# Optimization experiments

Hardware: AMD Instinct MI355X
Metric: run time of the kernel (lower is better)

Reference implementation:

```python
import jax, jax.numpy as jnp
import numpy as np

N, E = 16384, 65536
N2, A2, E2 = 65536, 131072, 262144
N3, A3, E3 = 65536, 196608, 262144
B = 256
F_IN, NI2, NI3 = 16, 64, 64


def setup_inputs() -> dict:
    key = jax.random.key(0)
    ks = iter(jax.random.split(key, 80))
    def rn(shape, s=1.0):
        return jax.random.normal(next(ks), shape, jnp.float32) * s
    def ru(shape):
        return jax.random.uniform(next(ks), shape, dtype=jnp.float32)
    def ri(shape, hi):
        return jax.random.randint(next(ks), shape, 0, hi)
    s = 0.05
    inp = {
        "x": rn((N, F_IN)),
        "edge_index": ri((2, E), N),
        "edge_attr": ru((E, 7)),
        "batch": jnp.sort(ri((N,), B)),
        "assign2_node": ri((A2,), N),
        "assign2_cluster": ri((A2,), N2),
        "iso_type_2": ru((N2, NI2)),
        "edge_index_2": ri((2, E2), N2),
        "batch_2": jnp.sort(ri((N2,), B)),
        "assign3_node": ri((A3,), N),
        "assign3_cluster": ri((A3,), N3),
        "iso_type_3": ru((N3, NI3)),
        "edge_index_3": ri((2, E3), N3),
        "batch_3": jnp.sort(ri((N3,), B)),
    }
    for i, (mi, mo) in enumerate([(F_IN, 32), (32, 64), (64, 64)], start=1):
        inp[f"nn{i}_W1"] = rn((7, 128), s)
        inp[f"nn{i}_b1"] = jnp.zeros((128,), jnp.float32)
        inp[f"nn{i}_W2"] = rn((128, mi * mo), s)
        inp[f"nn{i}_b2"] = jnp.zeros((mi * mo,), jnp.float32)
        inp[f"conv{i}_root"] = rn((mi, mo), s)
        inp[f"conv{i}_bias"] = jnp.zeros((mo,), jnp.float32)
    for i, din in zip([4, 5, 6, 7], [64 + NI2, 64, 64 + NI3, 64]):
        inp[f"conv{i}_Wrel"] = rn((din, 64), s)
        inp[f"conv{i}_Wroot"] = rn((din, 64), s)
        inp[f"conv{i}_bias"] = jnp.zeros((64,), jnp.float32)
    inp["fc1_W"] = rn((384, 64), s); inp["fc1_b"] = jnp.zeros((64,), jnp.float32)
    inp["fc2_W"] = rn((64, 32), s); inp["fc2_b"] = jnp.zeros((32,), jnp.float32)
    inp["fc3_W"] = rn((32, 1), s); inp["fc3_b"] = jnp.zeros((1,), jnp.float32)
    return inp


def nnconv(x, ei, ea, W1, b1, W2, b2, root, bias, mi, mo):
    # edge MLP -> per-edge [mi, mo] weight matrix; message = x_src @ W_e; scatter-add to dst
    h = jax.nn.relu(ea @ W1 + b1) @ W2 + b2          # [E, mi*mo]
    We = h.reshape(-1, mi, mo)
    msg = jnp.einsum('ei,eio->eo', x[ei[0]], We)     # [E, mo]
    agg = jax.ops.segment_sum(msg, ei[1], num_segments=x.shape[0])
    return x @ root + agg + bias


def graphconv(x, ei, Wrel, Wroot, bias):
    agg = jax.ops.segment_sum(x[ei[0]], ei[1], num_segments=x.shape[0])
    return agg @ Wrel + x @ Wroot + bias


def avg_pool_assign(x, node_idx, cluster_idx, num_clusters):
    s = jax.ops.segment_sum(x[node_idx], cluster_idx, num_segments=num_clusters)
    c = jax.ops.segment_sum(jnp.ones((node_idx.shape[0],), x.dtype), cluster_idx, num_segments=num_clusters)
    return s / jnp.clip(c, 1.0)[:, None]


def reference(x, edge_index, edge_attr, batch, assign2_node, assign2_cluster, iso_type_2, edge_index_2, batch_2, assign3_node, assign3_cluster, iso_type_3, edge_index_3, batch_3, nn1_W1, nn1_b1, nn1_W2, nn1_b2, conv1_root, conv1_bias, nn2_W1, nn2_b1, nn2_W2, nn2_b2, conv2_root, conv2_bias, nn3_W1, nn3_b1, nn3_W2, nn3_b2, conv3_root, conv3_bias, conv4_Wrel, conv4_Wroot, conv4_bias, conv5_Wrel, conv5_Wroot, conv5_bias, conv6_Wrel, conv6_Wroot, conv6_bias, conv7_Wrel, conv7_Wroot, conv7_bias, fc1_W, fc1_b, fc2_W, fc2_b, fc3_W, fc3_b):
    elu = jax.nn.elu
    h = elu(nnconv(x, edge_index, edge_attr, nn1_W1, nn1_b1, nn1_W2, nn1_b2, conv1_root, conv1_bias, F_IN, 32))
    h = elu(nnconv(h, edge_index, edge_attr, nn2_W1, nn2_b1, nn2_W2, nn2_b2, conv2_root, conv2_bias, 32, 64))
    h = elu(nnconv(h, edge_index, edge_attr, nn3_W1, nn3_b1, nn3_W2, nn3_b2, conv3_root, conv3_bias, 64, 64))
    x_1 = jax.ops.segment_sum(h, batch, num_segments=B)
    # 2-set level
    h2 = avg_pool_assign(h, assign2_node, assign2_cluster, N2)
    h2 = jnp.concatenate([h2, iso_type_2], axis=1)
    h2 = elu(graphconv(h2, edge_index_2, conv4_Wrel, conv4_Wroot, conv4_bias))
    h2 = elu(graphconv(h2, edge_index_2, conv5_Wrel, conv5_Wroot, conv5_bias))
    x_2 = jax.ops.segment_sum(h2, batch_2, num_segments=B)
    # 3-set level
    h3 = avg_pool_assign(h, assign3_node, assign3_cluster, N3)
    h3 = jnp.concatenate([h3, iso_type_3], axis=1)
    h3 = elu(graphconv(h3, edge_index_3, conv6_Wrel, conv6_Wroot, conv6_bias))
    h3 = elu(graphconv(h3, edge_index_3, conv7_Wrel, conv7_Wroot, conv7_bias))
    x_3 = jax.ops.segment_sum(h3, batch_3, num_segments=B)
    xc = jnp.concatenate([x_1, x_2, x_3], axis=1)
    xc = jnp.concatenate([xc, xc], axis=1)      # [B, 384]
    o = elu(xc @ fc1_W + fc1_b)
    o = elu(o @ fc2_W + fc2_b)
    o = o @ fc3_W + fc3_b
    return o.reshape(-1)
```

## Files before the change

### kernel.cpp

```cpp
#include <hip/hip_runtime.h>
#include <math.h>

#define NN 16384
#define E1N 65536
#define NBATCH 256
#define NC2 65536
#define KH 128
#define MNSTR 1092
#define OCS 136
#define ECAP 96

typedef _Float16 f16;
typedef _Float16 f16x2 __attribute__((ext_vector_type(2)));
typedef _Float16 f16x4 __attribute__((ext_vector_type(4)));
typedef _Float16 f16x8 __attribute__((ext_vector_type(8)));
typedef float    f32x4 __attribute__((ext_vector_type(4)));

__device__ __forceinline__ float elu1(float x){ return x > 0.f ? x : expm1f(x); }

__device__ __forceinline__ float dot2acc(f16x2 a, f16x2 b, float c){
#if __has_builtin(__builtin_amdgcn_fdot2)
  return __builtin_amdgcn_fdot2(a, b, c, false);
#else
  return fmaf((float)a[0], (float)b[0], fmaf((float)a[1], (float)b[1], c));
#endif
}

__global__ __launch_bounds__(256) void k_count(const int* __restrict__ arr, int* __restrict__ cnt, int n){
  int i = blockIdx.x*256 + threadIdx.x;
  if (i < n) atomicAdd(&cnt[arr[i]], 1);
}

__global__ __launch_bounds__(256) void k_scan1(const int* __restrict__ deg,
    int* __restrict__ ptr, int* __restrict__ partials){
  __shared__ int buf[256];
  int i = blockIdx.x*256 + threadIdx.x, t = threadIdx.x;
  int v = deg[i];
  buf[t] = v; __syncthreads();
  for (int o = 1; o < 256; o <<= 1){
    int x = (t >= o) ? buf[t-o] : 0;
    __syncthreads(); buf[t] += x; __syncthreads();
  }
  ptr[i] = buf[t] - v;
  if (t == 255) partials[blockIdx.x] = buf[255];
}

__global__ __launch_bounds__(256) void k_scan2(int* __restrict__ partials, int nb){
  __shared__ int buf[256];
  int t = threadIdx.x;
  int v = (t < nb) ? partials[t] : 0;
  buf[t] = v; __syncthreads();
  for (int o = 1; o < 256; o <<= 1){
    int x = (t >= o) ? buf[t-o] : 0;
    __syncthreads(); buf[t] += x; __syncthreads();
  }
  if (t < nb) partials[t] = buf[t] - v;
}

__global__ __launch_bounds__(256) void k_scan3(const int* __restrict__ partials,
    int* __restrict__ ptr, int* __restrict__ cur){
  int i = blockIdx.x*256 + threadIdx.x;
  int v = ptr[i] + partials[blockIdx.x];
  ptr[i] = v; cur[i] = v;
}

__global__ __launch_bounds__(256) void k_fill_edge(const int* __restrict__ ei, int* __restrict__ cursor,
    int* __restrict__ eids, int* __restrict__ srcs, int* __restrict__ dsts){
  int e = blockIdx.x*256 + threadIdx.x;
  if (e >= E1N) return;
  int s = ei[e];
  int p = atomicAdd(&cursor[s], 1);
  eids[p] = e; srcs[p] = s; dsts[p] = ei[E1N + e];
}

__global__ __launch_bounds__(256) void k_fill_dst(const int* __restrict__ eiL, int* __restrict__ cur,
    int* __restrict__ dsrc, int EL){
  int e = blockIdx.x*256 + threadIdx.x;
  if (e >= EL) return;
  int d = eiL[EL + e];
  int p = atomicAdd(&cur[d], 1);
  dsrc[p] = eiL[e];
}

__global__ __launch_bounds__(256) void k_fill_assign(const int* __restrict__ an, const int* __restrict__ ac,
    int* __restrict__ cur, int* __restrict__ an_sorted, int A){
  int a = blockIdx.x*256 + threadIdx.x;
  if (a >= A) return;
  int c = ac[a];
  int p = atomicAdd(&cur[c], 1);
  an_sorted[p] = an[a];
}

__global__ __launch_bounds__(256) void k_cvt16(const float* __restrict__ v, f16* __restrict__ o, int n){
  int t = blockIdx.x*256 + threadIdx.x;
  if (t < n) o[t] = (f16)v[t];
}

__global__ __launch_bounds__(256) void k_elu_both(float* __restrict__ v, f16* __restrict__ v16, int n){
  int t = blockIdx.x*256 + threadIdx.x;
  if (t < n){ float r = elu1(v[t]); v[t] = r; v16[t] = (f16)r; }
}

__global__ __launch_bounds__(256) void k_elu(float* __restrict__ v, int n){
  int t = blockIdx.x*256 + threadIdx.x;
  if (t < n) v[t] = elu1(v[t]);
}

__global__ __launch_bounds__(256) void k_packPrep(const float* __restrict__ root,
    const float* __restrict__ b2, f16* __restrict__ Bp, int mi, int mo, int S, int NB){
  int t = blockIdx.x*256 + threadIdx.x;
  if (t >= NB*S*512) return;
  int j = t & 7, l = (t >> 3) & 63, cs = t >> 9;
  int s = cs % S, c = cs / S;
  int k_in = s*32 + ((l>>4)<<3) + j;
  int n = c*16 + (l & 15);
  float v = 0.f;
  if (k_in < mi) v = (n < mo) ? root[k_in*mo + n] : b2[k_in*mo + (n - mo)];
  Bp[t] = (f16)v;
}

template<int MI, int S, int NB, int MO>
__global__ __launch_bounds__(256) void k_prep_mfma(const f16* __restrict__ A,
    const f16* __restrict__ Bp, const float* __restrict__ bias,
    float* __restrict__ outb, float* __restrict__ bterm){
  int l = threadIdx.x & 63, w = threadIdx.x >> 6;
  int r0 = blockIdx.x*64 + w*16;
  const f16* arow = A + (size_t)(r0 + (l & 15))*MI;
  f16x8 a[S];
  #pragma unroll
  for (int s=0;s<S;s++){
    int koff = s*32 + ((l>>4)<<3);
    if (koff < MI) a[s] = *(const f16x8*)(arow + koff);
    else           a[s] = (f16x8){0,0,0,0,0,0,0,0};
  }
  #pragma unroll
  for (int c=0;c<NB;c++){
    f32x4 acc = (f32x4){0.f,0.f,0.f,0.f};
    #pragma unroll
    for (int s=0;s<S;s++){
      f16x8 b = *(const f16x8*)(Bp + ((size_t)(c*S + s)*64 + l)*8);
      acc = __builtin_amdgcn_mfma_f32_16x16x32_f16(a[s], b, acc, 0, 0, 0);
    }
    int col = c*16 + (l & 15);
    #pragma unroll
    for (int r=0;r<4;r++){
      int row = r0 + ((l>>4)<<2) + r;
      if (col < MO) outb[(size_t)row*MO + col] = acc[r] + bias[col];
      else          bterm[(size_t)row*MO + (col - MO)] = acc[r];
    }
  }
}

__global__ __launch_bounds__(256) void k_w2pack_full(const float* __restrict__ W2,
    f16* __restrict__ Bp, int mi, int mo, int S){
  int t = blockIdx.x*256 + threadIdx.x;
  if (t >= mo*8*S*512) return;
  int j = t & 7, l = (t >> 3) & 63, cs = t >> 9;
  int s = cs % S, q = cs / S;
  int oc = q >> 3;
  int k  = (q & 7)*16 + (l & 15);
  int i  = s*32 + ((l>>4)<<3) + j;
  float v = (i < mi) ? W2[(size_t)k*mi*mo + (size_t)i*mo + oc] : 0.f;
  Bp[t] = (f16)v;
}

template<int MI, int S, int MO>
__global__ __launch_bounds__(256) void k_nnconv_fused3(const f16* __restrict__ xin16,
    const f16* __restrict__ W2p,
    const int* __restrict__ rowptr, const int* __restrict__ rowend,
    const int* __restrict__ srcs, const int* __restrict__ dsts,
    const int* __restrict__ eids,
    const float* __restrict__ ea, const float* __restrict__ W1,
    const float* __restrict__ b1,
    const float* __restrict__ bterm, float* __restrict__ outb){
  __shared__ __align__(16) f16   M[16*MNSTR];
  __shared__ __align__(16) f16   hb[ECAP*OCS];
  __shared__ __align__(16) float eas[ECAP*8];
  int t = threadIdx.x, l = t & 63, w = t >> 6;
  int n0 = blockIdx.x*16;
  int estart = rowptr[n0], eend = rowend[n0+15];
  if (estart >= eend) return;
  const f16* arow = xin16 + (size_t)(n0 + (l&15))*MI;
  f16x8 a[S];
  #pragma unroll
  for (int s=0;s<S;s++){
    int koff = s*32 + ((l>>4)<<3);
    if (koff < MI) a[s] = *(const f16x8*)(arow + koff);
    else           a[s] = (f16x8){0,0,0,0,0,0,0,0};
  }
  const int NCHUNK = MO/8;
  int oc = t & 7, eslot = t >> 3;
  for (int ebase = estart; ebase < eend; ebase += ECAP){
    int ecnt = eend - ebase; if (ecnt > ECAP) ecnt = ECAP;
    for (int idx = t; idx < ecnt*8; idx += 256){
      int e_ = idx >> 3, i = idx & 7;
      eas[idx] = (i < 7) ? ea[(size_t)eids[ebase + e_]*7 + i] : 0.f;
    }
    __syncthreads();
    for (int idx = t; idx < ecnt*32; idx += 256){
      int e_ = idx >> 5, p = idx & 31;
      int k0 = p*4;
      const float* xr = &eas[e_*8];
      float4 acc4 = *(const float4*)(b1 + k0);
      #pragma unroll
      for (int i=0;i<7;i++){
        float xv = xr[i];
        float4 wv = *(const float4*)(W1 + i*KH + k0);
        acc4.x = fmaf(xv, wv.x, acc4.x);
        acc4.y = fmaf(xv, wv.y, acc4.y);
        acc4.z = fmaf(xv, wv.z, acc4.z);
        acc4.w = fmaf(xv, wv.w, acc4.w);
      }
      f16x4 hv = { (f16)fmaxf(acc4.x,0.f), (f16)fmaxf(acc4.y,0.f),
                   (f16)fmaxf(acc4.z,0.f), (f16)fmaxf(acc4.w,0.f) };
      *(f16x4*)&hb[e_*OCS + k0] = hv;
    }
    __syncthreads();
    for (int c = 0; c < NCHUNK; c++){
      #pragma unroll
      for (int tt = 0; tt < 16; tt++){
        int q = c*64 + w*16 + tt;
        f32x4 acc = (f32x4){0.f,0.f,0.f,0.f};
        #pragma unroll
        for (int s=0;s<S;s++){
          f16x8 b = *(const f16x8*)(W2p + ((size_t)(q*S + s)*64 + l)*8);
          acc = __builtin_amdgcn_mfma_f32_16x16x32_f16(a[s], b, acc, 0, 0, 0);
        }
        int ocl = w*2 + (tt>>3);
        int kpos = (tt&7)*16 + (l & 15);
        f16* mp = &M[ocl*OCS + kpos];
        #pragma unroll
        for (int r=0;r<4;r++)
          mp[(size_t)(((l>>4)<<2) + r)*MNSTR] = (f16)acc[r];
      }
      __syncthreads();
      #pragma unroll
      for (int r2 = 0; r2 < ECAP/32; r2++){
        int ee = r2*32 + eslot;
        if (ee < ecnt){
          int e = ebase + ee;
          int s_ = srcs[e];
          int ln = s_ - n0;
          float acc = bterm[(size_t)s_*MO + c*8 + oc];
          const f16* mrow = &M[(size_t)ln*MNSTR + oc*OCS];
          const f16* hrow = &hb[ee*OCS];
          #pragma unroll 4
          for (int kk=0; kk<16; kk++){
            f16x8 h8 = *(const f16x8*)(hrow + kk*8);
            f16x4 m0 = *(const f16x4*)(mrow + kk*8);
            f16x4 m1 = *(const f16x4*)(mrow + kk*8 + 4);
            acc = dot2acc((f16x2){h8[0],h8[1]}, (f16x2){m0[0],m0[1]}, acc);
            acc = dot2acc((f16x2){h8[2],h8[3]}, (f16x2){m0[2],m0[3]}, acc);
            acc = dot2acc((f16x2){h8[4],h8[5]}, (f16x2){m1[0],m1[1]}, acc);
            acc = dot2acc((f16x2){h8[6],h8[7]}, (f16x2){m1[2],m1[3]}, acc);
          }
          atomicAdd(&outb[(size_t)dsts[e]*MO + c*8 + oc], acc);
        }
      }
      __syncthreads();
    }
  }
}

__global__ __launch_bounds__(256) void k_pool_gather(const int* __restrict__ aptr,
    const int* __restrict__ aend, const int* __restrict__ an_sorted,
    const float* __restrict__ h, const float* __restrict__ iso,
    f16* __restrict__ h16){
  int l = threadIdx.x & 63, w = threadIdx.x >> 6;
  int c = blockIdx.x*4 + w;
  int st = aptr[c], en = aend[c];
  float acc = 0.f;
  int e = st;
  for (; e+1 < en; e += 2){
    int n0 = an_sorted[e], n1 = an_sorted[e+1];
    acc += h[(size_t)n0*64 + l];
    acc += h[(size_t)n1*64 + l];
  }
  if (e < en) acc += h[(size_t)an_sorted[e]*64 + l];
  int cnt = en - st;
  float val = (cnt > 0) ? acc / (float)cnt : 0.f;
  h16[(size_t)c*128 + l] = (f16)val;
  h16[(size_t)c*128 + 64 + l] = (f16)iso[(size_t)c*64 + l];
}

__global__ __launch_bounds__(256) void k_packB_gc(const float* __restrict__ Wrel,
    const float* __restrict__ Wroot, f16* __restrict__ Bp, int S){
  int t = blockIdx.x*256 + threadIdx.x;
  if (t >= 8*S*512) return;
  int j = t & 7, l = (t >> 3) & 63, cs = t >> 9;
  int s = cs % S, c = cs / S;
  int k = s*32 + ((l>>4)<<3) + j;
  int n = (c<<4) + (l & 15);
  float v = (n < 64) ? Wrel[k*64 + n] : Wroot[k*64 + (n - 64)];
  Bp[t] = (f16)v;
}

template<int S>
__global__ __launch_bounds__(256) void k_gc_mfma(const f16* __restrict__ A,
    const f16* __restrict__ Bp, const float* __restrict__ bias,
    float* __restrict__ y, float* __restrict__ rbuf){
  int l = threadIdx.x & 63, w = threadIdx.x >> 6;
  int r0 = blockIdx.x*64 + w*16;
  const f16* arow = A + (size_t)(r0 + (l & 15))*(S*32);
  f16x8 a[S];
  #pragma unroll
  for (int s=0;s<S;s++) a[s] = *(const f16x8*)(arow + s*32 + ((l>>4)<<3));
  f32x4 acc[8];
  #pragma unroll
  for (int c=0;c<8;c++) acc[c] = (f32x4){0.f,0.f,0.f,0.f};
  #pragma unroll
  for (int c=0;c<8;c++){
    #pragma unroll
    for (int s=0;s<S;s++){
      f16x8 b = *(const f16x8*)(Bp + ((size_t)(c*S + s)*64 + l)*8);
      acc[c] = __builtin_amdgcn_mfma_f32_16x16x32_f16(a[s], b, acc[c], 0, 0, 0);
    }
  }
  #pragma unroll
  for (int c=0;c<8;c++){
    int col = c*16 + (l & 15);
    #pragma unroll
    for (int r=0;r<4;r++){
      int row = r0 + ((l>>4)<<2) + r;
      if (col < 64) y[(size_t)row*64 + col] = acc[c][r];
      else          rbuf[(size_t)row*64 + (col-64)] = acc[c][r] + bias[col-64];
    }
  }
}

template<bool F16OUT>
__global__ __launch_bounds__(256) void k_gc_gather(const int* __restrict__ dptr,
    const int* __restrict__ dend, const int* __restrict__ dsrc,
    const float* __restrict__ y, const float* __restrict__ rbuf,
    f16* __restrict__ o16, float* __restrict__ o32){
  int l = threadIdx.x & 63, w = threadIdx.x >> 6;
  int n = blockIdx.x*4 + w;
  int st = dptr[n], en = dend[n];
  float acc = rbuf[(size_t)n*64 + l];
  int e = st;
  for (; e+1 < en; e += 2){
    int s0 = dsrc[e], s1 = dsrc[e+1];
    acc += y[(size_t)s0*64 + l];
    acc += y[(size_t)s1*64 + l];
  }
  if (e < en) acc += y[(size_t)dsrc[e]*64 + l];
  float r = elu1(acc);
  if (F16OUT) o16[(size_t)n*64 + l] = (f16)r;
  else        o32[(size_t)n*64 + l] = r;
}

__device__ __forceinline__ int lowerb(const int* __restrict__ a, int n, int key){
  int lo = 0, hi = n;
  while (lo < hi){ int m = (lo + hi) >> 1; if (a[m] < key) lo = m + 1; else hi = m; }
  return lo;
}

__global__ __launch_bounds__(256) void k_batchsum_seg(const int* __restrict__ batch,
    const float* __restrict__ h, float* __restrict__ x123, int n_nodes, int off){
  __shared__ float red[4][64];
  int b = blockIdx.x;
  int lo = lowerb(batch, n_nodes, b);
  int hi = lowerb(batch, n_nodes, b+1);
  int col = threadIdx.x & 63, wq = threadIdx.x >> 6;
  float acc = 0.f;
  for (int n = lo + wq; n < hi; n += 4) acc += h[(size_t)n*64 + col];
  red[wq][col] = acc;
  __syncthreads();
  if (threadIdx.x < 64){
    float s = red[0][threadIdx.x] + red[1][threadIdx.x] + red[2][threadIdx.x] + red[3][threadIdx.x];
    x123[b*192 + off + threadIdx.x] = s;
  }
}

__global__ __launch_bounds__(256) void k_fc1(const float* __restrict__ x123,
    const float* __restrict__ W, const float* __restrict__ b, float* __restrict__ t1){
  int t = blockIdx.x*256 + threadIdx.x;
  if (t >= NBATCH*64) return;
  int bb = t >> 6, o = t & 63;
  const float* xr = x123 + bb*192;
  float acc = b[o];
  for (int j=0;j<192;j++) acc = fmaf(xr[j], W[j*64+o] + W[(192+j)*64+o], acc);
  t1[t] = elu1(acc);
}

__global__ __launch_bounds__(256) void k_fc2(const float* __restrict__ t1,
    const float* __restrict__ W, const float* __restrict__ b, float* __restrict__ t2){
  int t = blockIdx.x*256 + threadIdx.x;
  if (t >= NBATCH*32) return;
  int bb = t >> 5, o = t & 31;
  float acc = b[o];
  for (int j=0;j<64;j++) acc = fmaf(t1[bb*64+j], W[j*32+o], acc);
  t2[t] = elu1(acc);
}

__global__ __launch_bounds__(256) void k_fc3(const float* __restrict__ t2,
    const float* __restrict__ W, const float* __restrict__ b, float* __restrict__ out){
  int t = blockIdx.x*256 + threadIdx.x;
  if (t >= NBATCH) return;
  float acc = b[0];
  for (int j=0;j<32;j++) acc = fmaf(t2[t*32+j], W[j], acc);
  out[t] = acc;
}

static inline int cdiv(long long a, int b){ return (int)((a + b - 1) / b); }

extern "C" void kernel_launch(void* const* d_in, const int* in_sizes, int n_in,
                              void* d_out, int out_size, void* d_ws, size_t ws_size,
                              hipStream_t stream) {
  const float* x0    = (const float*)d_in[0];
  const int*   ei    = (const int*)d_in[1];
  const float* ea    = (const float*)d_in[2];
  const int*   batch = (const int*)d_in[3];
  const int*   a2n   = (const int*)d_in[4];
  const int*   a2c   = (const int*)d_in[5];
  const float* iso2  = (const float*)d_in[6];
  const int*   ei2   = (const int*)d_in[7];
  const int*   b2arr = (const int*)d_in[8];
  const int*   a3n   = (const int*)d_in[9];
  const int*   a3c   = (const int*)d_in[10];
  const float* iso3  = (const float*)d_in[11];
  const int*   ei3   = (const int*)d_in[12];
  const int*   b3arr = (const int*)d_in[13];
  const float* nnp[3][6];
  for (int c=0;c<3;c++) for (int p=0;p<6;p++) nnp[c][p] = (const float*)d_in[14 + 6*c + p];
  const float* c4W[3]; const float* c5W[3]; const float* c6W[3]; const float* c7W[3];
  for (int p=0;p<3;p++){ c4W[p]=(const float*)d_in[32+p]; c5W[p]=(const float*)d_in[35+p];
                         c6W[p]=(const float*)d_in[38+p]; c7W[p]=(const float*)d_in[41+p]; }
  const float* fc1W=(const float*)d_in[44]; const float* fc1b=(const float*)d_in[45];
  const float* fc2W=(const float*)d_in[46]; const float* fc2b=(const float*)d_in[47];
  const float* fc3W=(const float*)d_in[48]; const float* fc3b=(const float*)d_in[49];
  float* outp = (float*)d_out;

  char* ws = (char*)d_ws; size_t off = 0;
  auto alloc = [&](size_t bytes)->void*{ void* p = ws + off; off += (bytes + 255) & ~(size_t)255; return p; };
  const size_t SZ_R0 = (size_t)92*1024*1024;
  char* r0 = (char*)alloc(SZ_R0);
  f16*   W2p   = (f16*)r0;
  f16*   prepB = (f16*)(r0 + 2*1024*1024);
  float* bterm = (float*)(r0 + 2*1024*1024 + 64*1024);
  size_t o2 = 0;
  auto a2 = [&](size_t bytes)->char*{ char* p = r0 + o2; o2 += (bytes + 255) & ~(size_t)255; return p; };
  f16*   h16   = (f16*)  a2((size_t)NC2*128*2);
  float* ybuf  = (float*)a2((size_t)NC2*64*4);
  float* rbuf  = (float*)a2((size_t)NC2*64*4);
  float* gB    = (float*)a2((size_t)NC2*64*4);
  f16*   g16   = (f16*)  a2((size_t)NC2*64*2);
  f16*   BpGc  = (f16*)  a2((size_t)8*4*512*2);
  int*   aptr  = (int*)  a2((size_t)NC2*4);
  int*   acur  = (int*)  a2((size_t)NC2*4);
  int*   dptr  = (int*)  a2((size_t)NC2*4);
  int*   dcur  = (int*)  a2((size_t)NC2*4);
  int*   ldeg  = (int*)  a2((size_t)NC2*4);
  int*   ans   = (int*)  a2((size_t)196608*4);
  int*   dsrc  = (int*)  a2((size_t)262144*4);
  float* hA    = (float*)alloc((size_t)NN*32*4);
  float* hB    = (float*)alloc((size_t)NN*64*4);
  float* hC    = (float*)alloc((size_t)NN*64*4);
  f16*   x016  = (f16*)  alloc((size_t)NN*16*2);
  f16*   hA16  = (f16*)  alloc((size_t)NN*32*2);
  f16*   hB16  = (f16*)  alloc((size_t)NN*64*2);
  int*   deg   = (int*)  alloc((size_t)NN*4);
  int*   cursor= (int*)  alloc((size_t)NN*4);
  int*   rowptr= (int*)  alloc((size_t)NN*4);
  int*   eids  = (int*)  alloc((size_t)E1N*4);
  int*   srcs  = (int*)  alloc((size_t)E1N*4);
  int*   dsts  = (int*)  alloc((size_t)E1N*4);
  int*   parts = (int*)  alloc((size_t)256*4);
  float* x123  = (float*)alloc((size_t)NBATCH*192*4);
  float* t1    = (float*)alloc((size_t)NBATCH*64*4);
  float* t2    = (float*)alloc((size_t)NBATCH*32*4);
  (void)ws_size; (void)n_in; (void)in_sizes; (void)out_size;

  auto scan = [&](const int* dg, int n, int* ptr, int* cur){
    k_scan1<<<n/256,256,0,stream>>>(dg, ptr, parts);
    k_scan2<<<1,256,0,stream>>>(parts, n/256);
    k_scan3<<<n/256,256,0,stream>>>(parts, ptr, cur);
  };

  hipMemsetAsync(deg, 0, (size_t)NN*4, stream);
  k_count<<<cdiv(E1N,256),256,0,stream>>>(ei, deg, E1N);
  scan(deg, NN, rowptr, cursor);
  k_fill_edge<<<cdiv(E1N,256),256,0,stream>>>(ei, cursor, eids, srcs, dsts);
  k_cvt16<<<cdiv((long long)NN*16,256),256,0,stream>>>(x0, x016, NN*16);

  auto run_nnconv = [&](const f16* xin16, int mi, int mo,
                        const float* const* P, float* outb, f16* out16){
    const float* W1=P[0]; const float* b1=P[1]; const float* W2=P[2];
    const float* b2=P[3]; const float* root=P[4]; const float* bias=P[5];
    const int S = (mi > 32) ? 2 : 1;
    const int NB = (2*mo)/16;
    k_packPrep<<<cdiv((long long)NB*S*512,256),256,0,stream>>>(root, b2, prepB, mi, mo, S, NB);
    if (mi==16)      k_prep_mfma<16,1,4,32><<<NN/64,256,0,stream>>>(xin16, prepB, bias, outb, bterm);
    else if (mi==32) k_prep_mfma<32,1,8,64><<<NN/64,256,0,stream>>>(xin16, prepB, bias, outb, bterm);
    else             k_prep_mfma<64,2,8,64><<<NN/64,256,0,stream>>>(xin16, prepB, bias, outb, bterm);
    k_w2pack_full<<<cdiv((long long)mo*8*S*512,256),256,0,stream>>>(W2, W2p, mi, mo, S);
    if (mi==16)      k_nnconv_fused3<16,1,32><<<NN/16,256,0,stream>>>(xin16, W2p, rowptr, cursor, srcs, dsts, eids, ea, W1, b1, bterm, outb);
    else if (mi==32) k_nnconv_fused3<32,1,64><<<NN/16,256,0,stream>>>(xin16, W2p, rowptr, cursor, srcs, dsts, eids, ea, W1, b1, bterm, outb);
    else             k_nnconv_fused3<64,2,64><<<NN/16,256,0,stream>>>(xin16, W2p, rowptr, cursor, srcs, dsts, eids, ea, W1, b1, bterm, outb);
    if (out16) k_elu_both<<<cdiv((long long)NN*mo,256),256,0,stream>>>(outb, out16, NN*mo);
    else       k_elu<<<cdiv((long long)NN*mo,256),256,0,stream>>>(outb, NN*mo);
  };
  run_nnconv(x016, 16, 32, nnp[0], hA, hA16);
  run_nnconv(hA16, 32, 64, nnp[1], hB, hB16);
  run_nnconv(hB16, 64, 64, nnp[2], hC, nullptr);

  k_batchsum_seg<<<NBATCH,256,0,stream>>>(batch, hC, x123, NN, 0);

  auto run_level = [&](const int* an, const int* ac, int A, const float* iso,
                       const int* eiL, int EL, const int* batchL,
                       const float* const* cA, const float* const* cB, int off123){
    hipMemsetAsync(ldeg, 0, (size_t)NC2*4, stream);
    k_count<<<cdiv(A,256),256,0,stream>>>(ac, ldeg, A);
    scan(ldeg, NC2, aptr, acur);
    k_fill_assign<<<cdiv(A,256),256,0,stream>>>(an, ac, acur, ans, A);
    hipMemsetAsync(ldeg, 0, (size_t)NC2*4, stream);
    k_count<<<cdiv(EL,256),256,0,stream>>>(eiL + EL, ldeg, EL);
    scan(ldeg, NC2, dptr, dcur);
    k_fill_dst<<<cdiv(EL,256),256,0,stream>>>(eiL, dcur, dsrc, EL);
    k_pool_gather<<<NC2/4,256,0,stream>>>(aptr, acur, ans, hC, iso, h16);
    k_packB_gc<<<cdiv((long long)8*4*512,256),256,0,stream>>>(cA[0], cA[1], BpGc, 4);
    k_gc_mfma<4><<<NC2/64,256,0,stream>>>(h16, BpGc, cA[2], ybuf, rbuf);
    k_gc_gather<true><<<NC2/4,256,0,stream>>>(dptr, dcur, dsrc, ybuf, rbuf, g16, nullptr);
    k_packB_gc<<<cdiv((long long)8*2*512,256),256,0,stream>>>(cB[0], cB[1], BpGc, 2);
    k_gc_mfma<2><<<NC2/64,256,0,stream>>>(g16, BpGc, cB[2], ybuf, rbuf);
    k_gc_gather<false><<<NC2/4,256,0,stream>>>(dptr, dcur, dsrc, ybuf, rbuf, nullptr, gB);
    k_batchsum_seg<<<NBATCH,256,0,stream>>>(batchL, gB, x123, NC2, off123);
  };
  run_level(a2n, a2c, 131072, iso2, ei2, 262144, b2arr, c4W, c5W, 64);
  run_level(a3n, a3c, 196608, iso3, ei3, 262144, b3arr, c6W, c7W, 128);

  k_fc1<<<cdiv((long long)NBATCH*64,256),256,0,stream>>>(x123, fc1W, fc1b, t1);
  k_fc2<<<cdiv((long long)NBATCH*32,256),256,0,stream>>>(t1, fc2W, fc2b, t2);
  k_fc3<<<cdiv(NBATCH,256),256,0,stream>>>(t2, fc3W, fc3b, outp);
}
```

Baseline: 868.3 us.

## Replace atomic scatter with dst-CSR gather, batch levels, and move intermediates to fp16

The NNConv message kernel now writes per-edge fp16 messages instead of doing float atomic adds to destination nodes. A new destination-sorted gather kernel then sums those messages, adds the root term and applies ELU, which removes the separate ELU passes. The 2-set and 3-set levels are merged into dual kernels with combined counting, scanning, packing, GEMM and gather launches, and their intermediates are stored in fp16 to cut memory traffic. The per-node bterm rows are staged in shared memory. The cost is an extra message buffer and gather pass, plus lower precision in the stored intermediates.

```diff
diff --git a/kernel.cpp b/kernel.cpp
--- a/kernel.cpp
+++ b/kernel.cpp
@@ -5,9 +5,12 @@
 #define E1N 65536
 #define NBATCH 256
 #define NC2 65536
+#define A2N 131072
+#define A3N 196608
+#define ELV 262144
 #define KH 128
+#define OCS 136
 #define MNSTR 1092
-#define OCS 136
 #define ECAP 96
 
 typedef _Float16 f16;
@@ -24,11 +27,6 @@
 #else
   return fmaf((float)a[0], (float)b[0], fmaf((float)a[1], (float)b[1], c));
 #endif
-}
-
-__global__ __launch_bounds__(256) void k_count(const int* __restrict__ arr, int* __restrict__ cnt, int n){
-  int i = blockIdx.x*256 + threadIdx.x;
-  if (i < n) atomicAdd(&cnt[arr[i]], 1);
 }
 
 __global__ __launch_bounds__(256) void k_scan1(const int* __restrict__ deg,
@@ -45,16 +43,16 @@
   if (t == 255) partials[blockIdx.x] = buf[255];
 }
 
-__global__ __launch_bounds__(256) void k_scan2(int* __restrict__ partials, int nb){
+__global__ __launch_bounds__(256) void k_scan2seg(int* __restrict__ partials, int nb){
   __shared__ int buf[256];
-  int t = threadIdx.x;
-  int v = (t < nb) ? partials[t] : 0;
+  int t = threadIdx.x, base = blockIdx.x*nb;
+  int v = (t < nb) ? partials[base + t] : 0;
   buf[t] = v; __syncthreads();
   for (int o = 1; o < 256; o <<= 1){
     int x = (t >= o) ? buf[t-o] : 0;
     __syncthreads(); buf[t] += x; __syncthreads();
   }
-  if (t < nb) partials[t] = buf[t] - v;
+  if (t < nb) partials[base + t] = buf[t] - v;
 }
 
 __global__ __launch_bounds__(256) void k_scan3(const int* __restrict__ partials,
@@ -64,46 +62,65 @@
   ptr[i] = v; cur[i] = v;
 }
 
-__global__ __launch_bounds__(256) void k_fill_edge(const int* __restrict__ ei, int* __restrict__ cursor,
-    int* __restrict__ eids, int* __restrict__ srcs, int* __restrict__ dsts){
+__global__ __launch_bounds__(256) void k_count_edge_dual(const int* __restrict__ ei, int* __restrict__ deg){
   int e = blockIdx.x*256 + threadIdx.x;
   if (e >= E1N) return;
-  int s = ei[e];
-  int p = atomicAdd(&cursor[s], 1);
-  eids[p] = e; srcs[p] = s; dsts[p] = ei[E1N + e];
-}
-
-__global__ __launch_bounds__(256) void k_fill_dst(const int* __restrict__ eiL, int* __restrict__ cur,
-    int* __restrict__ dsrc, int EL){
+  atomicAdd(&deg[ei[e]], 1);
+  atomicAdd(&deg[NN + ei[E1N + e]], 1);
+}
+
+__global__ __launch_bounds__(256) void k_fill_edge_dual(const int* __restrict__ ei, int* __restrict__ cur,
+    int* __restrict__ eids, int* __restrict__ srcs, int* __restrict__ dpos){
   int e = blockIdx.x*256 + threadIdx.x;
-  if (e >= EL) return;
-  int d = eiL[EL + e];
-  int p = atomicAdd(&cur[d], 1);
-  dsrc[p] = eiL[e];
-}
-
-__global__ __launch_bounds__(256) void k_fill_assign(const int* __restrict__ an, const int* __restrict__ ac,
-    int* __restrict__ cur, int* __restrict__ an_sorted, int A){
-  int a = blockIdx.x*256 + threadIdx.x;
-  if (a >= A) return;
-  int c = ac[a];
-  int p = atomicAdd(&cur[c], 1);
-  an_sorted[p] = an[a];
+  if (e >= E1N) return;
+  int s = ei[e], d = ei[E1N + e];
+  int p = atomicAdd(&cur[s], 1);
+  eids[p] = e; srcs[p] = s;
+  int p2 = atomicAdd(&cur[NN + d], 1);
+  dpos[p2] = p;
+}
+
+__global__ __launch_bounds__(256) void k_count_assign_dual(const int* __restrict__ a2c,
+    const int* __restrict__ a3c, int* __restrict__ ldegA){
+  int i = blockIdx.x*256 + threadIdx.x;
+  if (i < A2N) atomicAdd(&ldegA[a2c[i]], 1);
+  else if (i < A2N + A3N) atomicAdd(&ldegA[NC2 + a3c[i - A2N]], 1);
+}
+
+__global__ __launch_bounds__(256) void k_fill_assign_dual(const int* __restrict__ a2n,
+    const int* __restrict__ a2c, const int* __restrict__ a3n, const int* __restrict__ a3c,
+    int* __restrict__ curA, int* __restrict__ ans2, int* __restrict__ ans3){
+  int i = blockIdx.x*256 + threadIdx.x;
+  if (i < A2N){
+    int p = atomicAdd(&curA[a2c[i]], 1); ans2[p] = a2n[i];
+  } else if (i < A2N + A3N){
+    int j = i - A2N;
+    int p = atomicAdd(&curA[NC2 + a3c[j]], 1); ans3[p] = a3n[j];
+  }
+}
+
+__global__ __launch_bounds__(256) void k_count_dst_dual(const int* __restrict__ ei2,
+    const int* __restrict__ ei3, int* __restrict__ ldegD){
+  int i = blockIdx.x*256 + threadIdx.x;
+  if (i < ELV) atomicAdd(&ldegD[ei2[ELV + i]], 1);
+  else if (i < 2*ELV) atomicAdd(&ldegD[NC2 + ei3[ELV + (i - ELV)]], 1);
+}
+
+__global__ __launch_bounds__(256) void k_fill_dst_dual(const int* __restrict__ ei2,
+    const int* __restrict__ ei3, int* __restrict__ curD,
+    int* __restrict__ dsrc2, int* __restrict__ dsrc3){
+  int i = blockIdx.x*256 + threadIdx.x;
+  if (i < ELV){
+    int p = atomicAdd(&curD[ei2[ELV + i]], 1); dsrc2[p] = ei2[i];
+  } else if (i < 2*ELV){
+    int j = i - ELV;
+    int p = atomicAdd(&curD[NC2 + ei3[ELV + j]], 1); dsrc3[p] = ei3[j];
+  }
 }
 
 __global__ __launch_bounds__(256) void k_cvt16(const float* __restrict__ v, f16* __restrict__ o, int n){
   int t = blockIdx.x*256 + threadIdx.x;
   if (t < n) o[t] = (f16)v[t];
-}
-
-__global__ __launch_bounds__(256) void k_elu_both(float* __restrict__ v, f16* __restrict__ v16, int n){
-  int t = blockIdx.x*256 + threadIdx.x;
-  if (t < n){ float r = elu1(v[t]); v[t] = r; v16[t] = (f16)r; }
-}
-
-__global__ __launch_bounds__(256) void k_elu(float* __restrict__ v, int n){
-  int t = blockIdx.x*256 + threadIdx.x;
-  if (t < n) v[t] = elu1(v[t]);
 }
 
 __global__ __launch_bounds__(256) void k_packPrep(const float* __restrict__ root,
@@ -122,7 +139,7 @@
 template<int MI, int S, int NB, int MO>
 __global__ __launch_bounds__(256) void k_prep_mfma(const f16* __restrict__ A,
     const f16* __restrict__ Bp, const float* __restrict__ bias,
-    float* __restrict__ outb, float* __restrict__ bterm){
+    float* __restrict__ prep, float* __restrict__ bterm){
   int l = threadIdx.x & 63, w = threadIdx.x >> 6;
   int r0 = blockIdx.x*64 + w*16;
   const f16* arow = A + (size_t)(r0 + (l & 15))*MI;
@@ -145,7 +162,7 @@
     #pragma unroll
     for (int r=0;r<4;r++){
       int row = r0 + ((l>>4)<<2) + r;
-      if (col < MO) outb[(size_t)row*MO + col] = acc[r] + bias[col];
+      if (col < MO) prep[(size_t)row*MO + col] = acc[r] + bias[col];
       else          bterm[(size_t)row*MO + (col - MO)] = acc[r];
     }
   }
@@ -165,21 +182,22 @@
 }
 
 template<int MI, int S, int MO>
-__global__ __launch_bounds__(256) void k_nnconv_fused3(const f16* __restrict__ xin16,
+__global__ __launch_bounds__(256) void k_nnconv_fused5(const f16* __restrict__ xin16,
     const f16* __restrict__ W2p,
     const int* __restrict__ rowptr, const int* __restrict__ rowend,
-    const int* __restrict__ srcs, const int* __restrict__ dsts,
-    const int* __restrict__ eids,
+    const int* __restrict__ srcs, const int* __restrict__ eids,
     const float* __restrict__ ea, const float* __restrict__ W1,
     const float* __restrict__ b1,
-    const float* __restrict__ bterm, float* __restrict__ outb){
+    const float* __restrict__ bterm, f16* __restrict__ msg16){
   __shared__ __align__(16) f16   M[16*MNSTR];
   __shared__ __align__(16) f16   hb[ECAP*OCS];
   __shared__ __align__(16) float eas[ECAP*8];
+  __shared__ float bt[16*MO];
   int t = threadIdx.x, l = t & 63, w = t >> 6;
   int n0 = blockIdx.x*16;
   int estart = rowptr[n0], eend = rowend[n0+15];
   if (estart >= eend) return;
+  for (int idx = t; idx < 16*MO; idx += 256) bt[idx] = bterm[(size_t)n0*MO + idx];
   const f16* arow = xin16 + (size_t)(n0 + (l&15))*MI;
   f16x8 a[S];
   #pragma unroll
@@ -241,7 +259,7 @@
           int e = ebase + ee;
           int s_ = srcs[e];
           int ln = s_ - n0;
-          float acc = bterm[(size_t)s_*MO + c*8 + oc];
+          float acc = bt[ln*MO + c*8 + oc];
           const f16* mrow = &M[(size_t)ln*MNSTR + oc*OCS];
           const f16* hrow = &hb[ee*OCS];
           #pragma unroll 4
@@ -254,7 +272,7 @@
             acc = dot2acc((f16x2){h8[4],h8[5]}, (f16x2){m1[0],m1[1]}, acc);
             acc = dot2acc((f16x2){h8[6],h8[7]}, (f16x2){m1[2],m1[3]}, acc);
           }
-          atomicAdd(&outb[(size_t)dsts[e]*MO + c*8 + oc], acc);
+          msg16[(size_t)e*MO + c*8 + oc] = (f16)acc;
         }
       }
       __syncthreads();
@@ -262,32 +280,71 @@
   }
 }
 
-__global__ __launch_bounds__(256) void k_pool_gather(const int* __restrict__ aptr,
-    const int* __restrict__ aend, const int* __restrict__ an_sorted,
-    const float* __restrict__ h, const float* __restrict__ iso,
+template<int MO>
+__global__ __launch_bounds__(256) void k_msg_gather(const int* __restrict__ dptr,
+    const int* __restrict__ dend, const int* __restrict__ dpos,
+    const f16* __restrict__ msg, const float* __restrict__ prep,
+    f16* __restrict__ out16){
+  int t = threadIdx.x, l = t & 63, w = t >> 6;
+  int n, o;
+  if (MO == 64){ n = blockIdx.x*4 + w; o = l; }
+  else         { n = blockIdx.x*8 + w*2 + (l>>5); o = l & 31; }
+  int st = dptr[n], en = dend[n];
+  float acc = prep[(size_t)n*MO + o];
+  int p = st;
+  for (; p+1 < en; p += 2){
+    int q0 = dpos[p], q1 = dpos[p+1];
+    acc += (float)msg[(size_t)q0*MO + o];
+    acc += (float)msg[(size_t)q1*MO + o];
+  }
+  if (p < en) acc += (float)msg[(size_t)dpos[p]*MO + o];
+  out16[(size_t)n*MO + o] = (f16)elu1(acc);
+}
+
+__global__ __launch_bounds__(256) void k_pool_gather_dual(const int* __restrict__ aptr,
+    const int* __restrict__ aend, const int* __restrict__ ans2, const int* __restrict__ ans3,
+    const f16* __restrict__ h, const float* __restrict__ iso2, const float* __restrict__ iso3,
     f16* __restrict__ h16){
   int l = threadIdx.x & 63, w = threadIdx.x >> 6;
-  int c = blockIdx.x*4 + w;
-  int st = aptr[c], en = aend[c];
+  int cg = blockIdx.x*4 + w;
+  int lvl = cg >= NC2;
+  int c = cg - lvl*NC2;
+  const int* ans = lvl ? ans3 : ans2;
+  const float* iso = lvl ? iso3 : iso2;
+  int st = aptr[cg], en = aend[cg];
   float acc = 0.f;
   int e = st;
   for (; e+1 < en; e += 2){
-    int n0 = an_sorted[e], n1 = an_sorted[e+1];
-    acc += h[(size_t)n0*64 + l];
-    acc += h[(size_t)n1*64 + l];
-  }
-  if (e < en) acc += h[(size_t)an_sorted[e]*64 + l];
+    int n0 = ans[e], n1 = ans[e+1];
+    acc += (float)h[(size_t)n0*64 + l];
+    acc += (float)h[(size_t)n1*64 + l];
+  }
+  if (e < en) acc += (float)h[(size_t)ans[e]*64 + l];
   int cnt = en - st;
   float val = (cnt > 0) ? acc / (float)cnt : 0.f;
-  h16[(size_t)c*128 + l] = (f16)val;
-  h16[(size_t)c*128 + 64 + l] = (f16)iso[(size_t)c*64 + l];
-}
-
-__global__ __launch_bounds__(256) void k_packB_gc(const float* __restrict__ Wrel,
-    const float* __restrict__ Wroot, f16* __restrict__ Bp, int S){
+  h16[(size_t)cg*128 + l] = (f16)val;
+  h16[(size_t)cg*128 + 64 + l] = (f16)iso[(size_t)c*64 + l];
+}
+
+#define BP_O4 0
+#define BP_O5 16384
+#define BP_O6 24576
+#define BP_O7 40960
+__global__ __launch_bounds__(256) void k_packB_all(
+    const float* __restrict__ W4r, const float* __restrict__ W4o,
+    const float* __restrict__ W5r, const float* __restrict__ W5o,
+    const float* __restrict__ W6r, const float* __restrict__ W6o,
+    const float* __restrict__ W7r, const float* __restrict__ W7o,
+    f16* __restrict__ Bp){
   int t = blockIdx.x*256 + threadIdx.x;
-  if (t >= 8*S*512) return;
-  int j = t & 7, l = (t >> 3) & 63, cs = t >> 9;
+  const float *Wrel, *Wroot; int S, base;
+  if      (t < BP_O5){ Wrel=W4r; Wroot=W4o; S=4; base=BP_O4; }
+  else if (t < BP_O6){ Wrel=W5r; Wroot=W5o; S=2; base=BP_O5; }
+  else if (t < BP_O7){ Wrel=W6r; Wroot=W6o; S=4; base=BP_O6; }
+  else if (t < 49152){ Wrel=W7r; Wroot=W7o; S=2; base=BP_O7; }
+  else return;
+  int u = t - base;
+  int j = u & 7, l = (u >> 3) & 63, cs = u >> 9;
   int s = cs % S, c = cs / S;
   int k = s*32 + ((l>>4)<<3) + j;
   int n = (c<<4) + (l & 15);
@@ -296,11 +353,20 @@
 }
 
 template<int S>
-__global__ __launch_bounds__(256) void k_gc_mfma(const f16* __restrict__ A,
-    const f16* __restrict__ Bp, const float* __restrict__ bias,
-    float* __restrict__ y, float* __restrict__ rbuf){
+__global__ __launch_bounds__(256) void k_gc_mfma_dual(const f16* __restrict__ Abase,
+    const f16* __restrict__ Bp, int bpo2, int bpo3,
+    const float* __restrict__ bias2, const float* __restrict__ bias3,
+    f16* __restrict__ y16, f16* __restrict__ rbuf16){
+  const int half = NC2/64;
+  int lvl = blockIdx.x >= half;
+  int bloc = blockIdx.x - lvl*half;
+  const f16* A = Abase + (size_t)lvl*NC2*(S*32);
+  const f16* B = Bp + (lvl ? bpo3 : bpo2);
+  const float* bias = lvl ? bias3 : bias2;
+  f16* y  = y16 + (size_t)lvl*NC2*64;
+  f16* rb = rbuf16 + (size_t)lvl*NC2*64;
   int l = threadIdx.x & 63, w = threadIdx.x >> 6;
-  int r0 = blockIdx.x*64 + w*16;
+  int r0 = bloc*64 + w*16;
   const f16* arow = A + (size_t)(r0 + (l & 15))*(S*32);
   f16x8 a[S];
   #pragma unroll
@@ -312,7 +378,7 @@
   for (int c=0;c<8;c++){
     #pragma unroll
     for (int s=0;s<S;s++){
-      f16x8 b = *(const f16x8*)(Bp + ((size_t)(c*S + s)*64 + l)*8);
+      f16x8 b = *(const f16x8*)(B + ((size_t)(c*S + s)*64 + l)*8);
       acc[c] = __builtin_amdgcn_mfma_f32_16x16x32_f16(a[s], b, acc[c], 0, 0, 0);
     }
   }
@@ -322,31 +388,34 @@
     #pragma unroll
     for (int r=0;r<4;r++){
       int row = r0 + ((l>>4)<<2) + r;
-      if (col < 64) y[(size_t)row*64 + col] = acc[c][r];
-      else          rbuf[(size_t)row*64 + (col-64)] = acc[c][r] + bias[col-64];
+      if (col < 64) y[(size_t)row*64 + col] = (f16)acc[c][r];
+      else          rb[(size_t)row*64 + (col-64)] = (f16)(acc[c][r] + bias[col-64]);
     }
   }
 }
 
-template<bool F16OUT>
-__global__ __launch_bounds__(256) void k_gc_gather(const int* __restrict__ dptr,
-    const int* __restrict__ dend, const int* __restrict__ dsrc,
-    const float* __restrict__ y, const float* __restrict__ rbuf,
-    f16* __restrict__ o16, float* __restrict__ o32){
+__global__ __launch_bounds__(256) void k_gc_gather_dual(const int* __restrict__ dptrD,
+    const int* __restrict__ dcurD, const int* __restrict__ dsrc2, const int* __restrict__ dsrc3,
+    const f16* __restrict__ y16, const f16* __restrict__ rbuf16,
+    f16* __restrict__ obase){
   int l = threadIdx.x & 63, w = threadIdx.x >> 6;
-  int n = blockIdx.x*4 + w;
-  int st = dptr[n], en = dend[n];
-  float acc = rbuf[(size_t)n*64 + l];
+  int ng = blockIdx.x*4 + w;
+  int lvl = ng >= NC2;
+  int n = ng - lvl*NC2;
+  const int* dsrc = lvl ? dsrc3 : dsrc2;
+  const f16* y  = y16 + (size_t)lvl*NC2*64;
+  const f16* rb = rbuf16 + (size_t)lvl*NC2*64;
+  f16* o = obase + (size_t)lvl*NC2*64;
+  int st = dptrD[ng], en = dcurD[ng];
+  float acc = (float)rb[(size_t)n*64 + l];
   int e = st;
   for (; e+1 < en; e += 2){
     int s0 = dsrc[e], s1 = dsrc[e+1];
-    acc += y[(size_t)s0*64 + l];
-    acc += y[(size_t)s1*64 + l];
-  }
-  if (e < en) acc += y[(size_t)dsrc[e]*64 + l];
-  float r = elu1(acc);
-  if (F16OUT) o16[(size_t)n*64 + l] = (f16)r;
-  else        o32[(size_t)n*64 + l] = r;
+    acc += (float)y[(size_t)s0*64 + l];
+    acc += (float)y[(size_t)s1*64 + l];
+  }
+  if (e < en) acc += (float)y[(size_t)dsrc[e]*64 + l];
+  o[(size_t)n*64 + l] = (f16)elu1(acc);
 }
 
 __device__ __forceinline__ int lowerb(const int* __restrict__ a, int n, int key){
@@ -355,20 +424,25 @@
   return lo;
 }
 
-__global__ __launch_bounds__(256) void k_batchsum_seg(const int* __restrict__ batch,
-    const float* __restrict__ h, float* __restrict__ x123, int n_nodes, int off){
+__global__ __launch_bounds__(256) void k_batchsum3(const int* __restrict__ b1,
+    const int* __restrict__ b2, const int* __restrict__ b3,
+    const f16* __restrict__ s1, const f16* __restrict__ s2, const f16* __restrict__ s3,
+    float* __restrict__ x123){
   __shared__ float red[4][64];
-  int b = blockIdx.x;
-  int lo = lowerb(batch, n_nodes, b);
-  int hi = lowerb(batch, n_nodes, b+1);
+  int seg = blockIdx.x >> 8, b = blockIdx.x & 255;
+  const int* batch = (seg==0) ? b1 : ((seg==1) ? b2 : b3);
+  const f16* src   = (seg==0) ? s1 : ((seg==1) ? s2 : s3);
+  int nn = (seg==0) ? NN : NC2;
+  int lo = lowerb(batch, nn, b);
+  int hi = lowerb(batch, nn, b+1);
   int col = threadIdx.x & 63, wq = threadIdx.x >> 6;
   float acc = 0.f;
-  for (int n = lo + wq; n < hi; n += 4) acc += h[(size_t)n*64 + col];
+  for (int n = lo + wq; n < hi; n += 4) acc += (float)src[(size_t)n*64 + col];
   red[wq][col] = acc;
   __syncthreads();
   if (threadIdx.x < 64){
     float s = red[0][threadIdx.x] + red[1][threadIdx.x] + red[2][threadIdx.x] + red[3][threadIdx.x];
-    x123[b*192 + off + threadIdx.x] = s;
+    x123[b*192 + seg*64 + threadIdx.x] = s;
   }
 }
 
@@ -438,97 +512,94 @@
   f16*   W2p   = (f16*)r0;
   f16*   prepB = (f16*)(r0 + 2*1024*1024);
   float* bterm = (float*)(r0 + 2*1024*1024 + 64*1024);
+  float* prep  = (float*)(r0 + 2*1024*1024 + 64*1024 + (size_t)NN*64*4);
+  f16*   msg16 = (f16*)  (r0 + 2*1024*1024 + 64*1024 + (size_t)NN*64*8);
   size_t o2 = 0;
   auto a2 = [&](size_t bytes)->char*{ char* p = r0 + o2; o2 += (bytes + 255) & ~(size_t)255; return p; };
-  f16*   h16   = (f16*)  a2((size_t)NC2*128*2);
-  float* ybuf  = (float*)a2((size_t)NC2*64*4);
-  float* rbuf  = (float*)a2((size_t)NC2*64*4);
-  float* gB    = (float*)a2((size_t)NC2*64*4);
-  f16*   g16   = (f16*)  a2((size_t)NC2*64*2);
-  f16*   BpGc  = (f16*)  a2((size_t)8*4*512*2);
-  int*   aptr  = (int*)  a2((size_t)NC2*4);
-  int*   acur  = (int*)  a2((size_t)NC2*4);
-  int*   dptr  = (int*)  a2((size_t)NC2*4);
-  int*   dcur  = (int*)  a2((size_t)NC2*4);
-  int*   ldeg  = (int*)  a2((size_t)NC2*4);
-  int*   ans   = (int*)  a2((size_t)196608*4);
-  int*   dsrc  = (int*)  a2((size_t)262144*4);
-  float* hA    = (float*)alloc((size_t)NN*32*4);
-  float* hB    = (float*)alloc((size_t)NN*64*4);
-  float* hC    = (float*)alloc((size_t)NN*64*4);
+  f16*   h16   = (f16*)  a2((size_t)2*NC2*128*2);
+  f16*   y16   = (f16*)  a2((size_t)2*NC2*64*2);
+  f16*   rbuf16= (f16*)  a2((size_t)2*NC2*64*2);
+  f16*   g16   = (f16*)  a2((size_t)2*NC2*64*2);
+  f16*   BpGc  = (f16*)  a2((size_t)49152*2);
+  int*   ldegA = (int*)  a2((size_t)4*NC2*4);
+  int*   ldegD = ldegA + 2*NC2;
+  int*   ptrA  = (int*)  a2((size_t)2*NC2*4);
+  int*   curA  = (int*)  a2((size_t)2*NC2*4);
+  int*   ptrD  = (int*)  a2((size_t)2*NC2*4);
+  int*   curD  = (int*)  a2((size_t)2*NC2*4);
+  int*   ans2  = (int*)  a2((size_t)A2N*4);
+  int*   ans3  = (int*)  a2((size_t)A3N*4);
+  int*   dsrc2 = (int*)  a2((size_t)ELV*4);
+  int*   dsrc3 = (int*)  a2((size_t)ELV*4);
+  f16*   fin2  = h16;
+  f16*   fin3  = h16 + (size_t)NC2*64;
   f16*   x016  = (f16*)  alloc((size_t)NN*16*2);
   f16*   hA16  = (f16*)  alloc((size_t)NN*32*2);
   f16*   hB16  = (f16*)  alloc((size_t)NN*64*2);
-  int*   deg   = (int*)  alloc((size_t)NN*4);
-  int*   cursor= (int*)  alloc((size_t)NN*4);
-  int*   rowptr= (int*)  alloc((size_t)NN*4);
+  f16*   hC16  = (f16*)  alloc((size_t)NN*64*2);
+  int*   deg1  = (int*)  alloc((size_t)2*NN*4);
+  int*   ptr1  = (int*)  alloc((size_t)2*NN*4);
+  int*   cur1  = (int*)  alloc((size_t)2*NN*4);
   int*   eids  = (int*)  alloc((size_t)E1N*4);
   int*   srcs  = (int*)  alloc((size_t)E1N*4);
-  int*   dsts  = (int*)  alloc((size_t)E1N*4);
-  int*   parts = (int*)  alloc((size_t)256*4);
+  int*   dpos  = (int*)  alloc((size_t)E1N*4);
+  int*   parts = (int*)  alloc((size_t)512*4);
   float* x123  = (float*)alloc((size_t)NBATCH*192*4);
   float* t1    = (float*)alloc((size_t)NBATCH*64*4);
   float* t2    = (float*)alloc((size_t)NBATCH*32*4);
   (void)ws_size; (void)n_in; (void)in_sizes; (void)out_size;
 
-  auto scan = [&](const int* dg, int n, int* ptr, int* cur){
-    k_scan1<<<n/256,256,0,stream>>>(dg, ptr, parts);
-    k_scan2<<<1,256,0,stream>>>(parts, n/256);
-    k_scan3<<<n/256,256,0,stream>>>(parts, ptr, cur);
+  auto scan = [&](const int* dg, int totalN, int segs, int* ptr, int* cur){
+    int nb = totalN/256/segs;
+    k_scan1<<<totalN/256,256,0,stream>>>(dg, ptr, parts);
+    k_scan2seg<<<segs,256,0,stream>>>(parts, nb);
+    k_scan3<<<totalN/256,256,0,stream>>>(parts, ptr, cur);
   };
 
-  hipMemsetAsync(deg, 0, (size_t)NN*4, stream);
-  k_count<<<cdiv(E1N,256),256,0,stream>>>(ei, deg, E1N);
-  scan(deg, NN, rowptr, cursor);
-  k_fill_edge<<<cdiv(E1N,256),256,0,stream>>>(ei, cursor, eids, srcs, dsts);
+  hipMemsetAsync(deg1, 0, (size_t)2*NN*4, stream);
+  k_count_edge_dual<<<cdiv(E1N,256),256,0,stream>>>(ei, deg1);
+  scan(deg1, 2*NN, 2, ptr1, cur1);
+  k_fill_edge_dual<<<cdiv(E1N,256),256,0,stream>>>(ei, cur1, eids, srcs, dpos);
   k_cvt16<<<cdiv((long long)NN*16,256),256,0,stream>>>(x0, x016, NN*16);
 
   auto run_nnconv = [&](const f16* xin16, int mi, int mo,
-                        const float* const* P, float* outb, f16* out16){
+                        const float* const* P, f16* out16){
     const float* W1=P[0]; const float* b1=P[1]; const float* W2=P[2];
     const float* b2=P[3]; const float* root=P[4]; const float* bias=P[5];
     const int S = (mi > 32) ? 2 : 1;
     const int NB = (2*mo)/16;
     k_packPrep<<<cdiv((long long)NB*S*512,256),256,0,stream>>>(root, b2, prepB, mi, mo, S, NB);
-    if (mi==16)      k_prep_mfma<16,1,4,32><<<NN/64,256,0,stream>>>(xin16, prepB, bias, outb, bterm);
-    else if (mi==32) k_prep_mfma<32,1,8,64><<<NN/64,256,0,stream>>>(xin16, prepB, bias, outb, bterm);
-    else             k_prep_mfma<64,2,8,64><<<NN/64,256,0,stream>>>(xin16, prepB, bias, outb, bterm);
+    if (mi==16)      k_prep_mfma<16,1,4,32><<<NN/64,256,0,stream>>>(xin16, prepB, bias, prep, bterm);
+    else if (mi==32) k_prep_mfma<32,1,8,64><<<NN/64,256,0,stream>>>(xin16, prepB, bias, prep, bterm);
+    else             k_prep_mfma<64,2,8,64><<<NN/64,256,0,stream>>>(xin16, prepB, bias, prep, bterm);
     k_w2pack_full<<<cdiv((long long)mo*8*S*512,256),256,0,stream>>>(W2, W2p, mi, mo, S);
-    if (mi==16)      k_nnconv_fused3<16,1,32><<<NN/16,256,0,stream>>>(xin16, W2p, rowptr, cursor, srcs, dsts, eids, ea, W1, b1, bterm, outb);
-    else if (mi==32) k_nnconv_fused3<32,1,64><<<NN/16,256,0,stream>>>(xin16, W2p, rowptr, cursor, srcs, dsts, eids, ea, W1, b1, bterm, outb);
-    else             k_nnconv_fused3<64,2,64><<<NN/16,256,0,stream>>>(xin16, W2p, rowptr, cursor, srcs, dsts, eids, ea, W1, b1, bterm, outb);
-    if (out16) k_elu_both<<<cdiv((long long)NN*mo,256),256,0,stream>>>(outb, out16, NN*mo);
-    else       k_elu<<<cdiv((long long)NN*mo,256),256,0,stream>>>(outb, NN*mo);
+    if (mi==16)      k_nnconv_fused5<16,1,32><<<NN/16,256,0,stream>>>(xin16, W2p, ptr1, cur1, srcs, eids, ea, W1, b1, bterm, msg16);
+    else if (mi==32) k_nnconv_fused5<32,1,64><<<NN/16,256,0,stream>>>(xin16, W2p, ptr1, cur1, srcs, eids, ea, W1, b1, bterm, msg16);
+    else             k_nnconv_fused5<64,2,64><<<NN/16,256,0,stream>>>(xin16, W2p, ptr1, cur1, srcs, eids, ea, W1, b1, bterm, msg16);
+    if (mo==32) k_msg_gather<32><<<NN/8,256,0,stream>>>(ptr1+NN, cur1+NN, dpos, msg16, prep, out16);
+    else        k_msg_gather<64><<<NN/4,256,0,stream>>>(ptr1+NN, cur1+NN, dpos, msg16, prep, out16);
   };
-  run_nnconv(x016, 16, 32, nnp[0], hA, hA16);
-  run_nnconv(hA16, 32, 64, nnp[1], hB, hB16);
-  run_nnconv(hB16, 64, 64, nnp[2], hC, nullptr);
-
-  k_batchsum_seg<<<NBATCH,256,0,stream>>>(batch, hC, x123, NN, 0);
-
-  auto run_level = [&](const int* an, const int* ac, int A, const float* iso,
-                       const int* eiL, int EL, const int* batchL,
-                       const float* const* cA, const float* const* cB, int off123){
-    hipMemsetAsync(ldeg, 0, (size_t)NC2*4, stream);
-    k_count<<<cdiv(A,256),256,0,stream>>>(ac, ldeg, A);
-    scan(ldeg, NC2, aptr, acur);
-    k_fill_assign<<<cdiv(A,256),256,0,stream>>>(an, ac, acur, ans, A);
-    hipMemsetAsync(ldeg, 0, (size_t)NC2*4, stream);
-    k_count<<<cdiv(EL,256),256,0,stream>>>(eiL + EL, ldeg, EL);
-    scan(ldeg, NC2, dptr, dcur);
-    k_fill_dst<<<cdiv(EL,256),256,0,stream>>>(eiL, dcur, dsrc, EL);
-    k_pool_gather<<<NC2/4,256,0,stream>>>(aptr, acur, ans, hC, iso, h16);
-    k_packB_gc<<<cdiv((long long)8*4*512,256),256,0,stream>>>(cA[0], cA[1], BpGc, 4);
-    k_gc_mfma<4><<<NC2/64,256,0,stream>>>(h16, BpGc, cA[2], ybuf, rbuf);
-    k_gc_gather<true><<<NC2/4,256,0,stream>>>(dptr, dcur, dsrc, ybuf, rbuf, g16, nullptr);
-    k_packB_gc<<<cdiv((long long)8*2*512,256),256,0,stream>>>(cB[0], cB[1], BpGc, 2);
-    k_gc_mfma<2><<<NC2/64,256,0,stream>>>(g16, BpGc, cB[2], ybuf, rbuf);
-    k_gc_gather<false><<<NC2/4,256,0,stream>>>(dptr, dcur, dsrc, ybuf, rbuf, nullptr, gB);
-    k_batchsum_seg<<<NBATCH,256,0,stream>>>(batchL, gB, x123, NC2, off123);
-  };
-  run_level(a2n, a2c, 131072, iso2, ei2, 262144, b2arr, c4W, c5W, 64);
-  run_level(a3n, a3c, 196608, iso3, ei3, 262144, b3arr, c6W, c7W, 128);
-
+  run_nnconv(x016, 16, 32, nnp[0], hA16);
+  run_nnconv(hA16, 32, 64, nnp[1], hB16);
+  run_nnconv(hB16, 64, 64, nnp[2], hC16);
+
+  hipMemsetAsync(ldegA, 0, (size_t)4*NC2*4, stream);
+  k_count_assign_dual<<<cdiv((long long)(A2N+A3N),256),256,0,stream>>>(a2c, a3c, ldegA);
+  scan(ldegA, 2*NC2, 2, ptrA, curA);
+  k_fill_assign_dual<<<cdiv((long long)(A2N+A3N),256),256,0,stream>>>(a2n, a2c, a3n, a3c, curA, ans2, ans3);
+  k_count_dst_dual<<<cdiv((long long)2*ELV,256),256,0,stream>>>(ei2, ei3, ldegD);
+  scan(ldegD, 2*NC2, 2, ptrD, curD);
+  k_fill_dst_dual<<<cdiv((long long)2*ELV,256),256,0,stream>>>(ei2, ei3, curD, dsrc2, dsrc3);
+
+  k_pool_gather_dual<<<2*NC2/4,256,0,stream>>>(ptrA, curA, ans2, ans3, hC16, iso2, iso3, h16);
+  k_packB_all<<<cdiv(49152,256),256,0,stream>>>(c4W[0], c4W[1], c5W[0], c5W[1],
+                                                c6W[0], c6W[1], c7W[0], c7W[1], BpGc);
+  k_gc_mfma_dual<4><<<2*NC2/64,256,0,stream>>>(h16, BpGc, BP_O4, BP_O6, c4W[2], c6W[2], y16, rbuf16);
+  k_gc_gather_dual<<<2*NC2/4,256,0,stream>>>(ptrD, curD, dsrc2, dsrc3, y16, rbuf16, g16);
+  k_gc_mfma_dual<2><<<2*NC2/64,256,0,stream>>>(g16, BpGc, BP_O5, BP_O7, c5W[2], c7W[2], y16, rbuf16);
+  k_gc_gather_dual<<<2*NC2/4,256,0,stream>>>(ptrD, curD, dsrc2, dsrc3, y16, rbuf16, fin2);
+
+  k_batchsum3<<<3*NBATCH,256,0,stream>>>(batch, b2arr, b3arr, hC16, fin2, fin3, x123);
   k_fc1<<<cdiv((long long)NBATCH*64,256),256,0,stream>>>(x123, fc1W, fc1b, t1);
   k_fc2<<<cdiv((long long)NBATCH*32,256),256,0,stream>>>(t1, fc2W, fc2b, t2);
   k_fc3<<<cdiv(NBATCH,256),256,0,stream>>>(t2, fc3W, fc3b, outp);
```

Measured after the change: 747.2 us. -13.9%, faster.
